# Performance work log

Hardware: AMD Instinct MI355X
Metric: run time of the kernel (lower is better)

## Reference

```python
import jax, jax.numpy as jnp
import numpy as np

K = 4  # top-k from init
BN_IS_FOLDED = True  # BatchNorm (eval mode) folded into per-channel scale s and shift t


def tconv(x, W):
    # x: (b, C, v, n); W: (Cout, Cin, 3) temporal conv, kernel (3,1,1), padding (1,0,0), no bias
    return jax.lax.conv_general_dilated(
        x, W[:, :, :, None], window_strides=(1, 1),
        padding=((1, 1), (0, 0)), dimension_numbers=('NCHW', 'OIHW', 'NCHW'))


def gcn_single(xn, src, dst, Wg, bg):
    # PyG GCNConv: add self-loops, symmetric normalization, then scatter-add.
    N = xn.shape[0]
    xl = xn @ Wg  # (N, C)
    loop = jnp.arange(N, dtype=src.dtype)
    s = jnp.concatenate([src, loop])
    d = jnp.concatenate([dst, loop])
    deg = jax.ops.segment_sum(jnp.ones(s.shape[0], dtype=xn.dtype), d, num_segments=N)
    dinv = jnp.where(deg > 0, jax.lax.rsqrt(deg), 0.0)
    norm = dinv[s] * dinv[d]
    out = jax.ops.segment_sum(norm[:, None] * xl[s], d, num_segments=N)
    return out + bg


def setup_inputs() -> dict:
    key = jax.random.key(0)
    ks = jax.random.split(key, 10)
    C = 256
    x = jax.random.normal(ks[0], (512, C, 16, 16), dtype=jnp.float32)
    Wd = jax.random.normal(ks[1], (C, C, 3), dtype=jnp.float32) * 0.02
    s1 = 1.0 + 0.1 * jax.random.normal(ks[2], (C,), dtype=jnp.float32)
    t1 = 0.1 * jax.random.normal(ks[3], (C,), dtype=jnp.float32)
    Wg = jax.random.normal(ks[4], (C, C), dtype=jnp.float32) * 0.02
    bg = 0.01 * jax.random.normal(ks[5], (C,), dtype=jnp.float32)
    Wu = jax.random.normal(ks[6], (C, C, 3), dtype=jnp.float32) * 0.02
    s2 = 1.0 + 0.1 * jax.random.normal(ks[7], (C,), dtype=jnp.float32)
    t2 = 0.1 * jax.random.normal(ks[8], (C,), dtype=jnp.float32)
    return {"x": x, "batch": 4, "Wd": Wd, "s1": s1, "t1": t1,
            "Wg": Wg, "bg": bg, "Wu": Wu, "s2": s2, "t2": t2}


def reference(x, batch, Wd, s1, t1, Wg, bg, Wu, s2, t2):
    tlen, c, h, w = x.shape
    b = batch
    v = tlen // b
    hw = h * w
    # (tlen,c,h,w) -> (b,c,v,h*w)
    x4 = x.reshape(b, v, c, h, w).transpose(0, 2, 1, 3, 4).reshape(b, c, v, hw)
    xd = tconv(x4, Wd) * s1[None, :, None, None] + t1[None, :, None, None]  # down_conv + BN(eval)

    # --- dynamic graph build (no-grad in original) ---
    f = jax.lax.stop_gradient(xd).transpose(0, 2, 3, 1)  # (b, v, hw, c)
    f1, f2 = f[:, :-1], f[:, 1:]                          # (b, t_1, hw, c)
    t_1 = v - 1
    sq1 = jnp.sum(f1 * f1, axis=-1)                       # (b,t_1,hw)
    sq2 = jnp.sum(f2 * f2, axis=-1)
    dots = jnp.einsum('btnc,btmc->btnm', f1, f2)
    d2 = jnp.maximum(sq1[..., :, None] + sq2[..., None, :] - 2.0 * dots, 0.0)
    sim = -jnp.sqrt(d2).reshape(b, t_1, hw * hw)
    sim = sim / jnp.maximum(jnp.linalg.norm(sim, axis=-1, keepdims=True), 1e-12)  # F.normalize
    sim = jnp.where(sim < 0.05, 100.0, sim)
    _, idx = jax.lax.top_k(sim, K)                        # (b, t_1, K)
    frame = jnp.arange(t_1, dtype=jnp.int32)[None, :, None]
    row = (idx // hw).astype(jnp.int32) + frame * hw
    col = (idx % hw).astype(jnp.int32) + (frame + 1) * hw
    row = row.reshape(b, -1)
    col = col.reshape(b, -1)
    src = jnp.concatenate([row, col], axis=1)             # forward + reversed edges
    dst = jnp.concatenate([col, row], axis=1)

    # --- per-sample GCN (batched with vmap) ---
    nodes = xd.transpose(0, 2, 3, 1).reshape(b, v * hw, c)  # 'b c v n -> b (v n) c'
    out = jax.vmap(lambda xn, s, d: gcn_single(xn, s, d, Wg, bg))(nodes, src, dst)

    # --- up path ---
    o4 = out.transpose(0, 2, 1).reshape(b, c, v, hw)
    xu = tconv(o4, Wu) * s2[None, :, None, None] + t2[None, :, None, None]
    return xu.reshape(b, c, v, h, w).transpose(0, 2, 1, 3, 4).reshape(tlen, c, h, w)
```

## Files before the change

### kernel.cpp

```cpp
#include <hip/hip_runtime.h>

typedef __attribute__((ext_vector_type(8))) short short8;
typedef __attribute__((ext_vector_type(4))) float f32x4;
typedef unsigned short u16;
typedef unsigned int u32;

#define FENCE() asm volatile("" ::: "memory")

__device__ __forceinline__ void gld_lds16(const void* g, void* l) {
  __builtin_amdgcn_global_load_lds((const __attribute__((address_space(1))) void*)g,
                                   (__attribute__((address_space(3))) void*)l,
                                   16, 0, 0);
}

__device__ __forceinline__ u16 f2b(float x) {
  union { float f; u32 u; } v; v.f = x;
  u32 u = v.u;
  return (u16)((u + 0x7FFFu + ((u >> 16) & 1u)) >> 16);
}
__device__ __forceinline__ float b2f(u16 x) {
  union { u32 u; float f; } v; v.u = ((u32)x) << 16; return v.f;
}
__device__ __forceinline__ u32 pack_pair(float lo, float hi) {
  return (u32)f2b(lo) | ((u32)f2b(hi) << 16);
}

__global__ __launch_bounds__(256) void k_pre(const float* __restrict__ x,
                                             const float* __restrict__ Wd, const float* __restrict__ Wg,
                                             const float* __restrict__ Wu,
                                             const float* __restrict__ s1, const float* __restrict__ t1,
                                             const float* __restrict__ bg,
                                             u16* __restrict__ xTz, u16* __restrict__ outz,
                                             u16* __restrict__ Wup, u16* __restrict__ Wcomb,
                                             float* __restrict__ c0, float* __restrict__ tWg) {
  __shared__ u16 tile[64][72];
  int blk = blockIdx.x;
  int tid = threadIdx.x;
  if (blk < 768) {
    int kk = blk >> 8;
    int ci = blk & 255;
    int j = tid;
    float a0 = 0.f, a1 = 0.f, a2 = 0.f, a3 = 0.f;
    for (int co = 0; co < 256; co += 4) {
      float w0 = b2f(f2b(Wg[(co + 0) * 256 + j] * s1[co + 0]));
      float w1 = b2f(f2b(Wg[(co + 1) * 256 + j] * s1[co + 1]));
      float w2 = b2f(f2b(Wg[(co + 2) * 256 + j] * s1[co + 2]));
      float w3 = b2f(f2b(Wg[(co + 3) * 256 + j] * s1[co + 3]));
      float d0 = b2f(f2b(Wd[(u32)(co + 0) * 768 + (u32)ci * 3 + kk]));
      float d1 = b2f(f2b(Wd[(u32)(co + 1) * 768 + (u32)ci * 3 + kk]));
      float d2 = b2f(f2b(Wd[(u32)(co + 2) * 768 + (u32)ci * 3 + kk]));
      float d3 = b2f(f2b(Wd[(u32)(co + 3) * 768 + (u32)ci * 3 + kk]));
      a0 = fmaf(w0, d0, a0);
      a1 = fmaf(w1, d1, a1);
      a2 = fmaf(w2, d2, a2);
      a3 = fmaf(w3, d3, a3);
    }
    Wcomb[(size_t)kk * 65536 + (size_t)j * 256 + ci] = f2b((a0 + a1) + (a2 + a3));
    return;
  }
  if (blk == 768) {
    int j = tid;
    float a0 = 0.f, a1 = 0.f, a2 = 0.f, a3 = 0.f;
    for (int co = 0; co < 256; co += 4) {
      a0 = fmaf(t1[co + 0], Wg[(co + 0) * 256 + j], a0);
      a1 = fmaf(t1[co + 1], Wg[(co + 1) * 256 + j], a1);
      a2 = fmaf(t1[co + 2], Wg[(co + 2) * 256 + j], a2);
      a3 = fmaf(t1[co + 3], Wg[(co + 3) * 256 + j], a3);
    }
    float a = (a0 + a1) + (a2 + a3);
    tWg[j] = a;
    c0[j] = a + bg[j];
    return;
  }
  if (blk < 1537) {
    int id = (blk - 769) * 256 + tid;
    int kk = id >> 16;
    int rem = id & 65535;
    int a = rem >> 8, b = rem & 255;
    Wup[id] = f2b(Wu[(u32)a * 768 + (u32)b * 3 + kk]);
    return;
  }
  if (blk < 1857) {
    int gid = (blk - 1537) * 256 + tid;
    int i = gid * 8;
    int buf = (i >= 327680) ? 1 : 0;
    int wi = i - buf * 327680;
    int f = wi >> 16;
    int off = wi & 65535;
    u16* dst = (buf ? xTz : outz) + (size_t)f * 129 * 65536 + off;
    *(uint4*)dst = make_uint4(0u, 0u, 0u, 0u);
    return;
  }
  int tblk = blk - 1857;
  int tl = tblk >> 4;
  int sub = tblk & 15;
  int ci0 = (sub >> 2) << 6;
  int p0 = (sub & 3) << 6;
  int i = tid >> 2;
  int ch = tid & 3;
  const float* gsrc = x + (size_t)tl * 65536 + (ci0 + i) * 256 + p0 + ch * 16;
  __align__(16) u16 cv[16];
#pragma unroll
  for (int v4 = 0; v4 < 4; ++v4) {
    float4 f = *(const float4*)(gsrc + v4 * 4);
    cv[v4 * 4 + 0] = f2b(f.x);
    cv[v4 * 4 + 1] = f2b(f.y);
    cv[v4 * 4 + 2] = f2b(f.z);
    cv[v4 * 4 + 3] = f2b(f.w);
  }
  *(uint4*)&tile[i][ch * 16] = *(const uint4*)&cv[0];
  *(uint4*)&tile[i][ch * 16 + 8] = *(const uint4*)&cv[8];
  __syncthreads();
  __align__(16) u16 tmp[16];
#pragma unroll
  for (int cc = 0; cc < 16; ++cc) tmp[cc] = tile[ch * 16 + cc][i];
  int fi = (tl >> 7) * 129 + (tl & 127) + 1;
  u16* gdst = xTz + (size_t)fi * 65536 + (p0 + i) * 256 + ci0 + ch * 16;
  *(uint4*)(gdst) = *(const uint4*)&tmp[0];
  *(uint4*)(gdst + 8) = *(const uint4*)&tmp[8];
}

__device__ __forceinline__ void store_pairs(u16* base, int row0, int stride, int colb,
                                            const float v[4], bool ev) {
  float pv[4];
#pragma unroll
  for (int r = 0; r < 4; ++r) pv[r] = __shfl_xor(v[r], 1, 64);
  u32 wd0 = ev ? pack_pair(v[0], pv[0]) : pack_pair(pv[0], v[0]);
  u32 wd1 = ev ? pack_pair(v[1], pv[1]) : pack_pair(pv[1], v[1]);
  u32 wd2 = ev ? pack_pair(v[2], pv[2]) : pack_pair(pv[2], v[2]);
  u32 wd3 = ev ? pack_pair(v[3], pv[3]) : pack_pair(pv[3], v[3]);
  u32 wa = ev ? wd0 : wd2;
  u32 wb = ev ? wd1 : wd3;
  int rs = ev ? 0 : 2;
  *(u32*)(base + (size_t)(row0 + rs) * stride + colb) = wa;
  *(u32*)(base + (size_t)(row0 + rs + 1) * stride + colb) = wb;
}

__device__ __forceinline__ void store_pairs_f32(float* base, int row0, int stride, int colb,
                                                const float v[4], bool ev) {
  float pv[4];
#pragma unroll
  for (int r = 0; r < 4; ++r) pv[r] = __shfl_xor(v[r], 1, 64);
  float2 wa, wb;
  if (ev) { wa = make_float2(v[0], pv[0]); wb = make_float2(v[1], pv[1]); }
  else    { wa = make_float2(pv[2], v[2]); wb = make_float2(pv[3], v[3]); }
  int rs = ev ? 0 : 2;
  *(float2*)(base + (size_t)(row0 + rs) * stride + colb) = wa;
  *(float2*)(base + (size_t)(row0 + rs + 1) * stride + colb) = wb;
}


__device__ __forceinline__ void stage_part(int s, const u16* Ab, const u16* Bb,
                                           u16* sA, u16* sB, int wuni, int g0) {
  if (s >= 48) return;
  const int tau = s >> 2;
  const int pt = s & 3;
  const int toff = ((tau >> 2) << 16) + ((tau & 3) << 6);
  const int half = pt & 1;
  const u16* src = ((pt & 2) ? Ab : Bb) + toff + (half << 15) + g0;
  u16* dst = ((pt & 2) ? sA : sB) + ((tau & 1) << 14) + (half << 13) + wuni;
  gld_lds16(src, dst);
  gld_lds16(src + 16384, dst + 4096);
}

template<int QUAD, int NH>
__device__ __forceinline__ void mfma_quad(f32x4 (&acc)[8][4], const short8 (&af)[2][4],
                                          const short8 (&bf)[2][2][2]) {
#pragma unroll
  for (int k = 0; k < 2; ++k)
#pragma unroll
    for (int m = 0; m < 4; ++m)
#pragma unroll
      for (int nj = 0; nj < 2; ++nj)
        acc[QUAD * 4 + m][NH * 2 + nj] = __builtin_amdgcn_mfma_f32_16x16x32_bf16(
            af[k][m], bf[NH][k][nj], acc[QUAD * 4 + m][NH * 2 + nj], 0, 0, 0);
}

__device__ __forceinline__ void gemm256_core(const u16* __restrict__ Ab, const u16* __restrict__ Bb,
                                             u16* sA, u16* sB, int tid, f32x4 (&acc)[8][4]) {
  const int lane = tid & 63;
  const int w = tid >> 6;
  const int wr = w >> 2;
  const int wc = w & 3;
  const int m16 = lane & 15;
  const int xorm = (lane & 7) << 4;
  const int q16b = (lane >> 4) << 4;
  const int koffe0 = ((q16b) ^ xorm) >> 1;
  const int koffe1 = ((64 + q16b) ^ xorm) >> 1;
  const int srow = tid >> 3;
  const int scol = ((tid & 7) ^ (srow & 7)) << 3;
  const int g0 = srow * 256 + scol;
  const int wuni = w << 9;

#pragma unroll
  for (int i = 0; i < 8; ++i)
#pragma unroll
    for (int j = 0; j < 4; ++j) acc[i][j] = (f32x4){0.f, 0.f, 0.f, 0.f};

#pragma unroll
  for (int s = 0; s < 7; ++s) stage_part(s, Ab, Bb, sA, sB, wuni, g0);
  asm volatile("s_waitcnt vmcnt(6)" ::: "memory");
  __builtin_amdgcn_s_barrier();
  FENCE();

  short8 af[2][4];
  short8 bf[2][2][2];
#pragma unroll 2
  for (int kt = 0; kt < 12; ++kt) {
    const int cb = kt & 1;
    const u16* aH = sA + cb * 16384 + wr * 8192;
    const u16* bH = sB + cb * 16384 + (wc >> 1) * 8192;
    const int bR0 = (wc & 1) << 6;
#pragma unroll
    for (int m = 0; m < 4; ++m) {
      const u16* p = aH + (m * 16 + m16) * 64;
      af[0][m] = *(const short8*)(p + koffe0);
      af[1][m] = *(const short8*)(p + koffe1);
    }
#pragma unroll
    for (int nh = 0; nh < 2; ++nh)
#pragma unroll
      for (int nj = 0; nj < 2; ++nj) {
        const u16* p = bH + (bR0 + (nh * 2 + nj) * 16 + m16) * 64;
        bf[nh][0][nj] = *(const short8*)(p + koffe0);
        bf[nh][1][nj] = *(const short8*)(p + koffe1);
      }
    stage_part(4 * kt + 7, Ab, Bb, sA, sB, wuni, g0);
    FENCE();
    __builtin_amdgcn_s_barrier();
    FENCE();
    __builtin_amdgcn_s_setprio(1);
    mfma_quad<0, 0>(acc, af, bf);
    __builtin_amdgcn_s_setprio(0);
    FENCE();
    __builtin_amdgcn_s_barrier();
    FENCE();
    stage_part(4 * kt + 8, Ab, Bb, sA, sB, wuni, g0);
    FENCE();
    __builtin_amdgcn_s_barrier();
    FENCE();
    __builtin_amdgcn_s_setprio(1);
    mfma_quad<0, 1>(acc, af, bf);
    __builtin_amdgcn_s_setprio(0);
    FENCE();
    __builtin_amdgcn_s_barrier();
    FENCE();
#pragma unroll
    for (int m = 0; m < 4; ++m) {
      const u16* p = aH + (64 + m * 16 + m16) * 64;
      af[0][m] = *(const short8*)(p + koffe0);
      af[1][m] = *(const short8*)(p + koffe1);
    }
    stage_part(4 * kt + 9, Ab, Bb, sA, sB, wuni, g0);
    FENCE();
    __builtin_amdgcn_s_barrier();
    FENCE();
    __builtin_amdgcn_s_setprio(1);
    mfma_quad<1, 0>(acc, af, bf);
    __builtin_amdgcn_s_setprio(0);
    FENCE();
    __builtin_amdgcn_s_barrier();
    FENCE();
    stage_part(4 * kt + 10, Ab, Bb, sA, sB, wuni, g0);
    FENCE();
    __builtin_amdgcn_s_barrier();
    FENCE();
    __builtin_amdgcn_s_setprio(1);
    mfma_quad<1, 1>(acc, af, bf);
    __builtin_amdgcn_s_setprio(0);
    if (kt < 10) asm volatile("s_waitcnt vmcnt(6)" ::: "memory");
    else         asm volatile("s_waitcnt vmcnt(0)" ::: "memory");
    __builtin_amdgcn_s_barrier();
    FENCE();
  }
}

__global__ __launch_bounds__(512, 2) void k_g12(const u16* __restrict__ xTz, const u16* __restrict__ Wcomb,
                                                const float* __restrict__ c0, const float* __restrict__ tWg,
                                                u16* __restrict__ outz, float* __restrict__ edge) {
  __shared__ u16 sA[32768];
  __shared__ u16 sB[32768];
  int bsw = (int)blockIdx.x;
  int bt = (bsw & 7) * 64 + (bsw >> 3);
  int b = bt >> 7, t = bt & 127;
  int tid = threadIdx.x;
  const u16* Ab = xTz + (size_t)(b * 129 + t) * 65536;
  const u16* Bb = Wcomb;
  f32x4 acc[8][4];
  gemm256_core(Ab, Bb, sA, sB, tid, acc);

  int lane = tid & 63, w = tid >> 6, wr = w >> 2, wc = w & 3;
  int q = lane >> 4, cc16 = lane & 15;
  bool ev = (lane & 1) == 0;
  float c0v[4], tWgv[4];
#pragma unroll
  for (int ni = 0; ni < 4; ++ni) {
    int j = wc * 64 + ni * 16 + cc16;
    c0v[ni] = c0[j];
    tWgv[ni] = tWg[j];
  }
  u16* obase = outz + (size_t)(b * 129 + t + 1) * 65536;
#pragma unroll
  for (int mi = 0; mi < 8; ++mi) {
    int row0 = wr * 128 + mi * 16 + q * 4;
#pragma unroll
    for (int ni = 0; ni < 4; ++ni) {
      float v[4];
#pragma unroll
      for (int r = 0; r < 4; ++r) v[r] = acc[mi][ni][r] + c0v[ni];
      store_pairs(obase, row0, 256, wc * 64 + ni * 16 + (cc16 & ~1), v, ev);
    }
  }
  if (wr == 0 && q == 0) {
    float* eb = edge + (size_t)bt * 1024;
#pragma unroll
    for (int ni = 0; ni < 4; ++ni) {
      float vE[4];
#pragma unroll
      for (int r = 0; r < 4; ++r) vE[r] = acc[0][ni][r] + tWgv[ni];
      store_pairs_f32(eb, 0, 256, wc * 64 + ni * 16 + (cc16 & ~1), vE, ev);
    }
  }
}

__device__ __forceinline__ float dinv0(int t) {
  if (t == 0) return 0.44721359549995793f;
  if (t == 127) return 0.7071067811865476f;
  return 0.4082482904638631f;
}
__global__ __launch_bounds__(256) void k_fix(const float* __restrict__ edge, const float* __restrict__ bg,
                                             u16* __restrict__ outz) {
  int bt = blockIdx.x;
  int b = bt >> 7;
  int t = bt & 127;
  int j = threadIdx.x;
  const float ISQ2 = 0.7071067811865476f;
  float bgv = bg[j];
  float e_t = edge[(size_t)bt * 1024 + j];
  float At = dinv0(t);
  float o0 = bgv + At * At * e_t;
  if (t <= 126) {
    float At1 = dinv0(t + 1);
    const float* en = edge + (size_t)(bt + 1) * 1024;
    float s = At1 * en[j] + ISQ2 * (en[256 + j] + en[512 + j] + en[768 + j]);
    o0 += At * s;
  }
  float em1 = 0.f, Atm1 = 0.f;
  if (t >= 1) {
    Atm1 = dinv0(t - 1);
    em1 = edge[(size_t)(bt - 1) * 1024 + j];
    o0 += At * Atm1 * em1;
  }
  u16* ob = outz + (size_t)(b * 129 + t + 1) * 65536;
  ob[j] = f2b(o0);
#pragma unroll
  for (int k = 1; k <= 3; ++k) {
    float m = edge[(size_t)bt * 1024 + k * 256 + j];
    float ok = (t == 0) ? (bgv + m) : (bgv + 0.5f * m + ISQ2 * Atm1 * em1);
    ob[k * 256 + j] = f2b(ok);
  }
}

__global__ __launch_bounds__(512, 2) void k_g3(const u16* __restrict__ outz, const u16* __restrict__ Wup,
                                               const float* __restrict__ s2, const float* __restrict__ t2,
                                               float* __restrict__ y) {
  __shared__ u16 sA[32768];
  __shared__ u16 sB[32768];
  int bsw = (int)blockIdx.x;
  int bt = (bsw & 7) * 64 + (bsw >> 3);
  int b = bt >> 7, t = bt & 127;
  int tid = threadIdx.x;
  const u16* Ab = Wup;
  const u16* Bb = outz + (size_t)(b * 129 + t) * 65536;
  f32x4 acc[8][4];
  gemm256_core(Ab, Bb, sA, sB, tid, acc);

  int lane = tid & 63, w = tid >> 6, wr = w >> 2, wc = w & 3;
  int q = lane >> 4, cc16 = lane & 15;
  bool ev = (lane & 1) == 0;
  float* ybase = y + (size_t)bt * 65536;
#pragma unroll
  for (int mi = 0; mi < 8; ++mi) {
    int rl = wr * 128 + mi * 16 + q * 4;
    float4 s4 = *(const float4*)(s2 + rl);
    float4 t4 = *(const float4*)(t2 + rl);
#pragma unroll
    for (int ni = 0; ni < 4; ++ni) {
      float v[4];
      v[0] = acc[mi][ni][0] * s4.x + t4.x;
      v[1] = acc[mi][ni][1] * s4.y + t4.y;
      v[2] = acc[mi][ni][2] * s4.z + t4.z;
      v[3] = acc[mi][ni][3] * s4.w + t4.w;
      store_pairs_f32(ybase, rl, 256, wc * 64 + ni * 16 + (cc16 & ~1), v, ev);
    }
  }
}

extern "C" void kernel_launch(void* const* d_in, const int* in_sizes, int n_in,
                              void* d_out, int out_size, void* d_ws, size_t ws_size,
                              hipStream_t stream) {
  (void)in_sizes; (void)n_in; (void)out_size; (void)ws_size;
  const float* x  = (const float*)d_in[0];
  const float* Wd = (const float*)d_in[2];
  const float* s1 = (const float*)d_in[3];
  const float* t1 = (const float*)d_in[4];
  const float* Wg = (const float*)d_in[5];
  const float* bg = (const float*)d_in[6];
  const float* Wu = (const float*)d_in[7];
  const float* s2 = (const float*)d_in[8];
  const float* t2 = (const float*)d_in[9];
  float* y = (float*)d_out;
  char* ws = (char*)d_ws;
  u16*   outz  = (u16*)(ws);
  u16*   xTz   = (u16*)(ws + 67764224);
  u16*   Wup   = (u16*)(ws + 136052736);
  u16*   Wcomb = (u16*)(ws + 136445952);
  float* c0    = (float*)(ws + 136839168);
  float* tWg   = (float*)(ws + 136840192);
  float* edge  = (float*)d_out;

  k_pre<<<dim3(10049), dim3(256), 0, stream>>>(x, Wd, Wg, Wu, s1, t1, bg, xTz, outz, Wup, Wcomb, c0, tWg);
  k_g12<<<dim3(512), dim3(512), 0, stream>>>(xTz, Wcomb, c0, tWg, outz, edge);
  k_fix<<<dim3(512), dim3(256), 0, stream>>>(edge, bg, outz);
  k_g3<<<dim3(512), dim3(512), 0, stream>>>(outz, Wup, s2, t2, y);
}
```

Baseline: 405.9 us.

## Fuse x fp32-to-bf16 transpose into first GEMM's A-tile staging

Removes the separate pre-pass that converted x to bf16, transposed it into a padded xTz buffer and zeroed its boundary frames. The GEMM kernel now loads fp32 x directly into registers, converts it with v_cvt_pk_bf16_f32, masks out-of-range temporal frames, and writes swizzled tiles into LDS inside its pipelined loop, while B tiles still use direct global-to-LDS loads. This avoids a full bf16 write and read-back of the activation. The cost is more register pressure and VALU work in the main loop, and occupancy drops because launch_bounds no longer requests 2 blocks per CU. The Wcomb precompute is also reworked to cache Wd and s1 in shared memory.

```diff
diff --git a/kernel.cpp b/kernel.cpp
--- a/kernel.cpp
+++ b/kernel.cpp
@@ -24,38 +24,41 @@
 __device__ __forceinline__ u32 pack_pair(float lo, float hi) {
   return (u32)f2b(lo) | ((u32)f2b(hi) << 16);
 }
-
-__global__ __launch_bounds__(256) void k_pre(const float* __restrict__ x,
-                                             const float* __restrict__ Wd, const float* __restrict__ Wg,
+__device__ __forceinline__ u32 cvtpk(float lo, float hi) {
+  u32 r;
+  asm("v_cvt_pk_bf16_f32 %0, %1, %2" : "=v"(r) : "v"(lo), "v"(hi));
+  return r;
+}
+__device__ __forceinline__ float fget(const float4& v, int r) {
+  switch (r) { case 0: return v.x; case 1: return v.y; case 2: return v.z; default: return v.w; }
+}
+
+__global__ __launch_bounds__(256) void k_pre(const float* __restrict__ Wd, const float* __restrict__ Wg,
                                              const float* __restrict__ Wu,
                                              const float* __restrict__ s1, const float* __restrict__ t1,
                                              const float* __restrict__ bg,
-                                             u16* __restrict__ xTz, u16* __restrict__ outz,
+                                             u16* __restrict__ outz,
                                              u16* __restrict__ Wup, u16* __restrict__ Wcomb,
                                              float* __restrict__ c0, float* __restrict__ tWg) {
-  __shared__ u16 tile[64][72];
+  __shared__ float wdv[256];
+  __shared__ float ws1[256];
   int blk = blockIdx.x;
   int tid = threadIdx.x;
   if (blk < 768) {
     int kk = blk >> 8;
     int ci = blk & 255;
     int j = tid;
-    float a0 = 0.f, a1 = 0.f, a2 = 0.f, a3 = 0.f;
-    for (int co = 0; co < 256; co += 4) {
-      float w0 = b2f(f2b(Wg[(co + 0) * 256 + j] * s1[co + 0]));
-      float w1 = b2f(f2b(Wg[(co + 1) * 256 + j] * s1[co + 1]));
-      float w2 = b2f(f2b(Wg[(co + 2) * 256 + j] * s1[co + 2]));
-      float w3 = b2f(f2b(Wg[(co + 3) * 256 + j] * s1[co + 3]));
-      float d0 = b2f(f2b(Wd[(u32)(co + 0) * 768 + (u32)ci * 3 + kk]));
-      float d1 = b2f(f2b(Wd[(u32)(co + 1) * 768 + (u32)ci * 3 + kk]));
-      float d2 = b2f(f2b(Wd[(u32)(co + 2) * 768 + (u32)ci * 3 + kk]));
-      float d3 = b2f(f2b(Wd[(u32)(co + 3) * 768 + (u32)ci * 3 + kk]));
-      a0 = fmaf(w0, d0, a0);
-      a1 = fmaf(w1, d1, a1);
-      a2 = fmaf(w2, d2, a2);
-      a3 = fmaf(w3, d3, a3);
-    }
-    Wcomb[(size_t)kk * 65536 + (size_t)j * 256 + ci] = f2b((a0 + a1) + (a2 + a3));
+    wdv[tid] = b2f(f2b(Wd[(u32)tid * 768 + (u32)ci * 3 + kk]));
+    ws1[tid] = s1[tid];
+    __syncthreads();
+    float a[8] = {0.f, 0.f, 0.f, 0.f, 0.f, 0.f, 0.f, 0.f};
+    for (int co = 0; co < 256; co += 8) {
+#pragma unroll
+      for (int u = 0; u < 8; ++u)
+        a[u] = fmaf(b2f(f2b(Wg[(co + u) * 256 + j] * ws1[co + u])), wdv[co + u], a[u]);
+    }
+    float s = ((a[0] + a[1]) + (a[2] + a[3])) + ((a[4] + a[5]) + (a[6] + a[7]));
+    Wcomb[(size_t)kk * 65536 + (size_t)j * 256 + ci] = f2b(s);
     return;
   }
   if (blk == 768) {
@@ -80,44 +83,12 @@
     Wup[id] = f2b(Wu[(u32)a * 768 + (u32)b * 3 + kk]);
     return;
   }
-  if (blk < 1857) {
-    int gid = (blk - 1537) * 256 + tid;
-    int i = gid * 8;
-    int buf = (i >= 327680) ? 1 : 0;
-    int wi = i - buf * 327680;
-    int f = wi >> 16;
-    int off = wi & 65535;
-    u16* dst = (buf ? xTz : outz) + (size_t)f * 129 * 65536 + off;
-    *(uint4*)dst = make_uint4(0u, 0u, 0u, 0u);
-    return;
-  }
-  int tblk = blk - 1857;
-  int tl = tblk >> 4;
-  int sub = tblk & 15;
-  int ci0 = (sub >> 2) << 6;
-  int p0 = (sub & 3) << 6;
-  int i = tid >> 2;
-  int ch = tid & 3;
-  const float* gsrc = x + (size_t)tl * 65536 + (ci0 + i) * 256 + p0 + ch * 16;
-  __align__(16) u16 cv[16];
-#pragma unroll
-  for (int v4 = 0; v4 < 4; ++v4) {
-    float4 f = *(const float4*)(gsrc + v4 * 4);
-    cv[v4 * 4 + 0] = f2b(f.x);
-    cv[v4 * 4 + 1] = f2b(f.y);
-    cv[v4 * 4 + 2] = f2b(f.z);
-    cv[v4 * 4 + 3] = f2b(f.w);
-  }
-  *(uint4*)&tile[i][ch * 16] = *(const uint4*)&cv[0];
-  *(uint4*)&tile[i][ch * 16 + 8] = *(const uint4*)&cv[8];
-  __syncthreads();
-  __align__(16) u16 tmp[16];
-#pragma unroll
-  for (int cc = 0; cc < 16; ++cc) tmp[cc] = tile[ch * 16 + cc][i];
-  int fi = (tl >> 7) * 129 + (tl & 127) + 1;
-  u16* gdst = xTz + (size_t)fi * 65536 + (p0 + i) * 256 + ci0 + ch * 16;
-  *(uint4*)(gdst) = *(const uint4*)&tmp[0];
-  *(uint4*)(gdst + 8) = *(const uint4*)&tmp[8];
+  int gid = (blk - 1537) * 256 + tid;
+  int i = gid * 8;
+  int f = i >> 16;
+  int off = i & 65535;
+  u16* dst = outz + (size_t)f * 129 * 65536 + off;
+  *(uint4*)dst = make_uint4(0u, 0u, 0u, 0u);
 }
 
 __device__ __forceinline__ void store_pairs(u16* base, int row0, int stride, int colb,
@@ -148,7 +119,6 @@
   *(float2*)(base + (size_t)(row0 + rs) * stride + colb) = wa;
   *(float2*)(base + (size_t)(row0 + rs + 1) * stride + colb) = wb;
 }
-
 
 __device__ __forceinline__ void stage_part(int s, const u16* Ab, const u16* Bb,
                                            u16* sA, u16* sB, int wuni, int g0) {
@@ -275,22 +245,159 @@
   }
 }
 
-__global__ __launch_bounds__(512, 2) void k_g12(const u16* __restrict__ xTz, const u16* __restrict__ Wcomb,
-                                                const float* __restrict__ c0, const float* __restrict__ tWg,
-                                                u16* __restrict__ outz, float* __restrict__ edge) {
+__global__ __launch_bounds__(512) void k_g12(const float* __restrict__ x, const u16* __restrict__ Wcomb,
+                                             const float* __restrict__ c0, const float* __restrict__ tWg,
+                                             u16* __restrict__ outz, float* __restrict__ edge) {
   __shared__ u16 sA[32768];
   __shared__ u16 sB[32768];
   int bsw = (int)blockIdx.x;
   int bt = (bsw & 7) * 64 + (bsw >> 3);
   int b = bt >> 7, t = bt & 127;
   int tid = threadIdx.x;
-  const u16* Ab = xTz + (size_t)(b * 129 + t) * 65536;
-  const u16* Bb = Wcomb;
+  const int lane = tid & 63;
+  const int w = tid >> 6;
+  const int wr = w >> 2, wc = w & 3;
+  const int m16 = lane & 15;
+  const int xorm = (lane & 7) << 4;
+  const int q16b = (lane >> 4) << 4;
+  const int koffe0 = (q16b ^ xorm) >> 1;
+  const int koffe1 = ((64 + q16b) ^ xorm) >> 1;
+  const int gAx = (((lane >> 2) & 3) ^ ((lane & 3) << 1)) << 4;
+  const int kA00 = (q16b ^ gAx) >> 1;
+  const int kA01 = ((q16b ^ gAx) ^ 64) >> 1;
+  const int kA10 = (((64 | q16b) ^ gAx)) >> 1;
+  const int kA11 = (((64 | q16b) ^ gAx) ^ 64) >> 1;
+  const int srow = tid >> 3;
+  const int scol = ((tid & 7) ^ (srow & 7)) << 3;
+  const int g0 = srow * 256 + scol;
+  const int wuni = w << 9;
+  const int o = w, q = lane;
+  const int qpart = (q & 3) ^ (((q >> 2) & 1) << 2);
+
+  float4 rf[8];
+
+  auto issueA = [&](int tau) {
+    int fr = tau >> 2, c = tau & 3;
+    int ft = t - 1 + fr;
+    int ftc = ft < 0 ? 0 : (ft > 127 ? 127 : ft);
+    const float* xb = x + ((size_t)(b * 128 + ftc)) * 65536 + (size_t)(c * 64 + o * 8) * 256 + (q << 2);
+#pragma unroll
+    for (int k = 0; k < 8; ++k) rf[k] = *(const float4*)(xb + k * 256);
+  };
+  auto cvtwrA = [&](int tau) {
+    int ft = t - 1 + (tau >> 2);
+    u32 msk = (ft >= 0 && ft <= 127) ? 0xFFFFFFFFu : 0u;
+    u16* sAd = sA + ((tau & 1) << 14);
+#pragma unroll
+    for (int r = 0; r < 4; ++r) {
+      u32 w0 = cvtpk(fget(rf[0], r), fget(rf[1], r)) & msk;
+      u32 w1 = cvtpk(fget(rf[2], r), fget(rf[3], r)) & msk;
+      u32 w2 = cvtpk(fget(rf[4], r), fget(rf[5], r)) & msk;
+      u32 w3 = cvtpk(fget(rf[6], r), fget(rf[7], r)) & msk;
+      *(uint4*)(sAd + (4 * q + r) * 64 + ((o ^ qpart ^ (r << 1)) << 3)) = make_uint4(w0, w1, w2, w3);
+    }
+  };
+  auto stageB = [&](int tau, int half) {
+    const int toff = ((tau >> 2) << 16) + ((tau & 3) << 6);
+    const u16* src = Wcomb + toff + (half << 15) + g0;
+    u16* dst = sB + ((tau & 1) << 14) + (half << 13) + wuni;
+    gld_lds16(src, dst);
+    gld_lds16(src + 16384, dst + 4096);
+  };
+
   f32x4 acc[8][4];
-  gemm256_core(Ab, Bb, sA, sB, tid, acc);
-
-  int lane = tid & 63, w = tid >> 6, wr = w >> 2, wc = w & 3;
-  int q = lane >> 4, cc16 = lane & 15;
+#pragma unroll
+  for (int i = 0; i < 8; ++i)
+#pragma unroll
+    for (int j = 0; j < 4; ++j) acc[i][j] = (f32x4){0.f, 0.f, 0.f, 0.f};
+
+  issueA(0);
+  asm volatile("s_waitcnt vmcnt(0)" ::: "memory");
+  cvtwrA(0);
+  stageB(0, 0); stageB(0, 1);
+  __builtin_amdgcn_sched_barrier(0);
+  stageB(1, 0); stageB(1, 1);
+  __builtin_amdgcn_sched_barrier(0);
+  issueA(1);
+  __builtin_amdgcn_sched_barrier(0);
+  asm volatile("s_waitcnt vmcnt(12)" ::: "memory");
+  asm volatile("s_waitcnt lgkmcnt(0)" ::: "memory");
+  __builtin_amdgcn_s_barrier();
+  FENCE();
+
+  short8 af[2][4];
+  short8 bf[2][2][2];
+#pragma unroll 2
+  for (int kt = 0; kt < 12; ++kt) {
+    const int cb = kt & 1;
+    const u16* aH = sA + cb * 16384 + wr * 8192;
+    const u16* bH = sB + cb * 16384 + (wc >> 1) * 8192;
+    const int bR0 = (wc & 1) << 6;
+#pragma unroll
+    for (int m = 0; m < 4; ++m) {
+      const u16* p = aH + (m * 16 + m16) * 64;
+      af[0][m] = *(const short8*)(p + ((m & 1) ? kA01 : kA00));
+      af[1][m] = *(const short8*)(p + ((m & 1) ? kA11 : kA10));
+    }
+#pragma unroll
+    for (int nh = 0; nh < 2; ++nh)
+#pragma unroll
+      for (int nj = 0; nj < 2; ++nj) {
+        const u16* p = bH + (bR0 + (nh * 2 + nj) * 16 + m16) * 64;
+        bf[nh][0][nj] = *(const short8*)(p + koffe0);
+        bf[nh][1][nj] = *(const short8*)(p + koffe1);
+      }
+    FENCE();
+    __builtin_amdgcn_s_barrier();
+    FENCE();
+    __builtin_amdgcn_s_setprio(1);
+    mfma_quad<0, 0>(acc, af, bf);
+    __builtin_amdgcn_s_setprio(0);
+    FENCE();
+    __builtin_amdgcn_s_barrier();
+    FENCE();
+    if (kt < 10) stageB(kt + 2, 0);
+    FENCE();
+    __builtin_amdgcn_s_barrier();
+    FENCE();
+    __builtin_amdgcn_s_setprio(1);
+    mfma_quad<0, 1>(acc, af, bf);
+    __builtin_amdgcn_s_setprio(0);
+    FENCE();
+    __builtin_amdgcn_s_barrier();
+    FENCE();
+#pragma unroll
+    for (int m = 0; m < 4; ++m) {
+      const u16* p = aH + (64 + m * 16 + m16) * 64;
+      af[0][m] = *(const short8*)(p + ((m & 1) ? kA01 : kA00));
+      af[1][m] = *(const short8*)(p + ((m & 1) ? kA11 : kA10));
+    }
+    if (kt < 10)       asm volatile("s_waitcnt vmcnt(2)" ::: "memory");
+    else if (kt == 10) asm volatile("s_waitcnt vmcnt(0)" ::: "memory");
+    if (kt < 11) cvtwrA(kt + 1);
+    if (kt < 10) {
+      stageB(kt + 2, 1);
+      __builtin_amdgcn_sched_barrier(0);
+      issueA(kt + 2);
+    }
+    FENCE();
+    __builtin_amdgcn_s_barrier();
+    FENCE();
+    __builtin_amdgcn_s_setprio(1);
+    mfma_quad<1, 0>(acc, af, bf);
+    __builtin_amdgcn_s_setprio(0);
+    FENCE();
+    __builtin_amdgcn_s_barrier();
+    FENCE();
+    __builtin_amdgcn_s_setprio(1);
+    mfma_quad<1, 1>(acc, af, bf);
+    __builtin_amdgcn_s_setprio(0);
+    asm volatile("s_waitcnt lgkmcnt(0)" ::: "memory");
+    __builtin_amdgcn_s_barrier();
+    FENCE();
+  }
+
+  int qf = lane >> 4, cc16 = lane & 15;
   bool ev = (lane & 1) == 0;
   float c0v[4], tWgv[4];
 #pragma unroll
@@ -302,7 +409,7 @@
   u16* obase = outz + (size_t)(b * 129 + t + 1) * 65536;
 #pragma unroll
   for (int mi = 0; mi < 8; ++mi) {
-    int row0 = wr * 128 + mi * 16 + q * 4;
+    int row0 = wr * 128 + mi * 16 + qf * 4;
 #pragma unroll
     for (int ni = 0; ni < 4; ++ni) {
       float v[4];
@@ -311,7 +418,7 @@
       store_pairs(obase, row0, 256, wc * 64 + ni * 16 + (cc16 & ~1), v, ev);
     }
   }
-  if (wr == 0 && q == 0) {
+  if (wr == 0 && qf == 0) {
     float* eb = edge + (size_t)bt * 1024;
 #pragma unroll
     for (int ni = 0; ni < 4; ++ni) {
@@ -412,15 +519,14 @@
   float* y = (float*)d_out;
   char* ws = (char*)d_ws;
   u16*   outz  = (u16*)(ws);
-  u16*   xTz   = (u16*)(ws + 67764224);
-  u16*   Wup   = (u16*)(ws + 136052736);
-  u16*   Wcomb = (u16*)(ws + 136445952);
-  float* c0    = (float*)(ws + 136839168);
-  float* tWg   = (float*)(ws + 136840192);
+  u16*   Wup   = (u16*)(ws + 67764224);
+  u16*   Wcomb = (u16*)(ws + 68157440);
+  float* c0    = (float*)(ws + 68550656);
+  float* tWg   = (float*)(ws + 68551680);
   float* edge  = (float*)d_out;
 
-  k_pre<<<dim3(10049), dim3(256), 0, stream>>>(x, Wd, Wg, Wu, s1, t1, bg, xTz, outz, Wup, Wcomb, c0, tWg);
-  k_g12<<<dim3(512), dim3(512), 0, stream>>>(xTz, Wcomb, c0, tWg, outz, edge);
+  k_pre<<<dim3(1697), dim3(256), 0, stream>>>(Wd, Wg, Wu, s1, t1, bg, outz, Wup, Wcomb, c0, tWg);
+  k_g12<<<dim3(512), dim3(512), 0, stream>>>(x, Wcomb, c0, tWg, outz, edge);
   k_fix<<<dim3(512), dim3(256), 0, stream>>>(edge, bg, outz);
   k_g3<<<dim3(512), dim3(512), 0, stream>>>(outz, Wup, s2, t2, y);
 }
```

After: 416.1 us. 1.03x slower.
